# Optimization experiments

Hardware: AMD Instinct MI355X
Metric: run time of the kernel (lower is better)

## Reference

```python
import jax, jax.numpy as jnp
import numpy as np

B, T, F_IN = 32, 1664, 80
H_ENC, KV, D_DEC, EMB, VOCAB, L_DEC = 256, 128, 512, 256, 30, 200
SOS = 0  # letter2index['<sos>']


def _cell(x, h, c, Wih, Whh, b):
    # PyTorch LSTMCell gate order: i, f, g, o
    g = x @ Wih.T + h @ Whh.T + b
    i, f, gg, o = jnp.split(g, 4, axis=-1)
    c = jax.nn.sigmoid(f) * c + jax.nn.sigmoid(i) * jnp.tanh(gg)
    h = jax.nn.sigmoid(o) * jnp.tanh(c)
    return h, c


def _lstm(x, Wih, Whh, b):  # x: [B, T, D] -> [B, T, H]
    Bq, H = x.shape[0], Whh.shape[1]
    z = jnp.zeros((Bq, H), x.dtype)

    def step(hc, xt):
        h, c = _cell(xt, hc[0], hc[1], Wih, Whh, b)
        return (h, c), h

    _, hs = jax.lax.scan(step, (z, z), jnp.swapaxes(x, 0, 1))
    return jnp.swapaxes(hs, 0, 1)


def _bilstm(x, fWih, fWhh, fb, bWih, bWhh, bb):
    fw = _lstm(x, fWih, fWhh, fb)
    bw = _lstm(x[:, ::-1], bWih, bWhh, bb)[:, ::-1]
    return jnp.concatenate([fw, bw], axis=-1)


def _forward(floats, x_len, y):
    (x, e_fw_Wih, e_fw_Whh, e_fw_b, e_bw_Wih, e_bw_Whh, e_bw_b,
     p_fw_Wih, p_fw_Whh, p_fw_b, p_bw_Wih, p_bw_Whh, p_bw_b,
     Wk, bk, Wv, bv, emb, d1_Wih, d1_Whh, d1_b, d2_Wih, d2_Whh, d2_b, b_out) = floats

    # ---- Encoder: biLSTM + 3 pyramidal biLSTMs ('concat' trunc) ----
    out = _bilstm(x, e_fw_Wih, e_fw_Whh, e_fw_b, e_bw_Wih, e_bw_Whh, e_bw_b)  # [B,T,512]
    for i in range(3):
        Bn, Tn, Dn = out.shape
        out = out[:, :(Tn // 2) * 2].reshape(Bn, Tn // 2, Dn * 2)  # concat pairs of frames
        out = _bilstm(out, p_fw_Wih[i], p_fw_Whh[i], p_fw_b[i],
                      p_bw_Wih[i], p_bw_Whh[i], p_bw_b[i])
    key_ = out @ Wk.T + bk   # [B, S, KV]
    val = out @ Wv.T + bv    # [B, S, KV]
    S = key_.shape[1]

    enc_len = x_len // 8  # three halvings
    mask = jnp.arange(S)[None, :] < enc_len[:, None]  # [B, S]
    scale = 1.0 / np.sqrt(KV).astype(np.float32)

    def attend(q):  # q: [B, KV]
        e = jnp.einsum('bd,bsd->bs', q, key_) * scale
        e = jnp.where(mask, e, jnp.finfo(e.dtype).min)
        a = jax.nn.softmax(e, axis=-1)
        ctx = jnp.einsum('bs,bsd->bd', a, val)
        return ctx, a

    # ---- Decoder (train mode, teacher_forcing_rate == 1) ----
    ctx0, _ = attend(jnp.zeros((B, KV), x.dtype))
    emb_seq = emb[y]                                    # [B, L, EMB]
    sos = jnp.broadcast_to(emb[SOS], (B, EMB))
    ins = jnp.concatenate([sos[:, None], emb_seq[:, :-1]], axis=1)  # input at step t
    z1 = jnp.zeros((B, D_DEC), x.dtype)
    z2 = jnp.zeros((B, KV), x.dtype)

    def step(st, et):
        h1, c1, h2, c2, ctx = st
        yc = jnp.concatenate([et, ctx], axis=-1)
        h1, c1 = _cell(yc, h1, c1, d1_Wih, d1_Whh, d1_b)
        h2, c2 = _cell(h1, h2, c2, d2_Wih, d2_Whh, d2_b)
        ctx, a = attend(h2)
        logits = jnp.concatenate([h2, ctx], axis=-1) @ emb.T + b_out  # tied weights
        return (h1, c1, h2, c2, ctx), (logits, a[0])

    _, (logits, attn0) = jax.lax.scan(step, (z1, z1, z2, z2, ctx0), jnp.swapaxes(ins, 0, 1))
    predictions = jnp.swapaxes(logits, 0, 1)  # [B, L, VOCAB]
    return predictions, attn0                 # attn0: [L, S] (attention of sample 0)


def setup_inputs() -> dict:
    key = jax.random.key(0)
    ks = iter(jax.random.split(key, 40))

    def p(shape):
        return jax.random.normal(next(ks), shape, dtype=jnp.float32) * 0.05

    d = {
        'x': jax.random.normal(next(ks), (B, T, F_IN), dtype=jnp.float32),
        'x_len': jnp.full((B,), T, dtype=jnp.int32),
        'y': jax.random.randint(next(ks), (B, L_DEC), 0, VOCAB),
        # encoder base biLSTM (in=80, hid=256)
        'e_fw_Wih': p((4 * H_ENC, F_IN)), 'e_fw_Whh': p((4 * H_ENC, H_ENC)), 'e_fw_b': p((4 * H_ENC,)),
        'e_bw_Wih': p((4 * H_ENC, F_IN)), 'e_bw_Whh': p((4 * H_ENC, H_ENC)), 'e_bw_b': p((4 * H_ENC,)),
        # 3 pBLSTMs (in=1024 concat, hid=256), stacked on leading axis
        'p_fw_Wih': p((3, 4 * H_ENC, 4 * H_ENC)), 'p_fw_Whh': p((3, 4 * H_ENC, H_ENC)), 'p_fw_b': p((3, 4 * H_ENC)),
        'p_bw_Wih': p((3, 4 * H_ENC, 4 * H_ENC)), 'p_bw_Whh': p((3, 4 * H_ENC, H_ENC)), 'p_bw_b': p((3, 4 * H_ENC)),
        'Wk': p((KV, 2 * H_ENC)), 'bk': p((KV,)),
        'Wv': p((KV, 2 * H_ENC)), 'bv': p((KV,)),
        'emb': p((VOCAB, EMB)),  # tied with character_prob weight (EMB == 2*KV)
        'd1_Wih': p((4 * D_DEC, EMB + KV)), 'd1_Whh': p((4 * D_DEC, D_DEC)), 'd1_b': p((4 * D_DEC,)),
        'd2_Wih': p((4 * KV, D_DEC)), 'd2_Whh': p((4 * KV, KV)), 'd2_b': p((4 * KV,)),
        'b_out': p((VOCAB,)),
    }
    return d


def reference(x, e_fw_Wih, e_fw_Whh, e_fw_b, e_bw_Wih, e_bw_Whh, e_bw_b,
              p_fw_Wih, p_fw_Whh, p_fw_b, p_bw_Wih, p_bw_Whh, p_bw_b,
              Wk, bk, Wv, bv, emb, d1_Wih, d1_Whh, d1_b, d2_Wih, d2_Whh, d2_b, b_out,
              x_len, y):
    floats = (x, e_fw_Wih, e_fw_Whh, e_fw_b, e_bw_Wih, e_bw_Whh, e_bw_b,
              p_fw_Wih, p_fw_Whh, p_fw_b, p_bw_Wih, p_bw_Whh, p_bw_b,
              Wk, bk, Wv, bv, emb, d1_Wih, d1_Whh, d1_b, d2_Wih, d2_Whh, d2_b, b_out)
    return _forward(floats, x_len, y)
```

## Files before the change

kernel.cpp:

```cpp
#include <hip/hip_runtime.h>
#include <hip/hip_bf16.h>
#include <math.h>
#include <stdint.h>


#define DEV __device__ __forceinline__

#define FLAG_STRIDE 16

DEV float sigmf(float x) { return 1.0f / (1.0f + __expf(-x)); }
DEV float tanh_(float x) { return 1.0f - 2.0f / (__expf(2.0f * x) + 1.0f); }

struct __align__(8) bf4 { __hip_bfloat16 a, b, c, d; };

DEV float4 ld4g(const float* p) { return *(const float4*)p; }
DEV float4 ld4g(const __hip_bfloat16* p) {
    bf4 v = *(const bf4*)p;
    return make_float4(__bfloat162float(v.a), __bfloat162float(v.b),
                       __bfloat162float(v.c), __bfloat162float(v.d));
}
DEV void st1g(float* p, float v) { *p = v; }
DEV void st1g(__hip_bfloat16* p, float v) { *p = __float2bfloat16(v); }

DEV void st_coh(float* p, float v) {
    __hip_atomic_store(p, v, __ATOMIC_RELAXED, __HIP_MEMORY_SCOPE_AGENT);
}
DEV unsigned long long ld_coh64(const unsigned long long* p) {
    return __hip_atomic_load(p, __ATOMIC_RELAXED, __HIP_MEMORY_SCOPE_AGENT);
}
DEV float ld_coh32(const float* p) {
    return __hip_atomic_load(p, __ATOMIC_RELAXED, __HIP_MEMORY_SCOPE_AGENT);
}
DEV void st_coh64(unsigned long long* p, unsigned long long v) {
    __hip_atomic_store(p, v, __ATOMIC_RELAXED, __HIP_MEMORY_SCOPE_AGENT);
}

extern __shared__ float dyn_pad[];

DEV void step_barrier(unsigned* myflags, int w, int tid, unsigned tv)
{
    __syncthreads();
    if (tid == 0)
        __hip_atomic_store(&myflags[w * FLAG_STRIDE], tv, __ATOMIC_RELAXED,
                           __HIP_MEMORY_SCOPE_AGENT);
    if (tid < 128) {
        int guard = 0;
        while (__hip_atomic_load(&myflags[tid * FLAG_STRIDE], __ATOMIC_RELAXED,
                                 __HIP_MEMORY_SCOPE_AGENT) < tv) {
            __builtin_amdgcn_s_sleep(1);
            if (++guard > (1 << 15)) break;
        }
    }
    __syncthreads();
}

template <typename ST>
__global__ __launch_bounds__(256, 1) void lstm_l0(
    const float* __restrict__ x,
    const float* __restrict__ whh_f, const float* __restrict__ whh_b,
    const float* __restrict__ wih_f, const float* __restrict__ wih_b,
    const float* __restrict__ bias_f, const float* __restrict__ bias_b,
    ST* __restrict__ out,
    float* __restrict__ hbuf, unsigned* __restrict__ flags)
{
    const int T = 1664;
    const int RS = 388;
    __shared__ __align__(16) float hs[32 * 388];
    __shared__ float pb[4][32][9];

    const int tid = threadIdx.x;
    const int dir = blockIdx.x >> 7;
    const int w = blockIdx.x & 127;
    const int wave = tid >> 6, lane = tid & 63;
    const int cl = lane & 7;
    const int ksub = lane >> 3;
    const int slot = (wave * 8 + ksub) * 4;
    const int col = (cl >> 1) * 256 + w * 2 + (cl & 1);

    const float* Whh = dir ? whh_b : whh_f;
    const float* Wih = dir ? wih_b : wih_f;
    const float* bias = dir ? bias_b : bias_f;

    float4 wreg[3];
#pragma unroll
    for (int c = 0; c < 3; c++) {
        int k = c * 128 + slot;
        float4 v = make_float4(0.f, 0.f, 0.f, 0.f);
        if (k < 256) v = *(const float4*)&Whh[(size_t)col * 256 + k];
        else if (k - 256 < 80) v = *(const float4*)&Wih[(size_t)col * 80 + (k - 256)];
        wreg[c] = v;
    }

    const int qb = tid >> 1, qj = tid & 1;
    float bias_g[4];
#pragma unroll
    for (int g = 0; g < 4; g++) bias_g[g] = bias[g * 256 + w * 2 + (tid & 1)];
    float c_reg = 0.f;

    unsigned* myflags = flags + dir * 128 * FLAG_STRIDE;
    float* hb_base = hbuf + dir * 2 * 8192;

    for (int i = tid; i < 32 * 52; i += 256)
        hs[(i / 52) * RS + 336 + (i % 52)] = 0.f;

    for (int t = 0; t < T; t++) {
        const int par = t & 1;
        const int t_act = dir ? (T - 1 - t) : t;
        const unsigned long long* h64 =
            (const unsigned long long*)(hb_base + par * 8192);

        unsigned long long hv64[16];
#pragma unroll
        for (int j = 0; j < 16; j++)
            hv64[j] = ld_coh64(&h64[tid + j * 256]);
        float4 xf[3];
        int xn = 0;
        for (int i4 = tid; i4 < 640; i4 += 256) {
            int e = i4 * 4;
            xf[xn++] = *(const float4*)&x[((size_t)(e / 80) * 1664 + t_act) * 80 + (e % 80)];
        }
#pragma unroll
        for (int j = 0; j < 16; j++) {
            int q = tid + j * 256;
            int u = q >> 4, b0 = (q & 15) * 2;
            int uc = u ^ ((q & 7) << 2);
            hs[b0 * RS + uc] = __uint_as_float((unsigned)hv64[j]);
            hs[(b0 + 1) * RS + uc] = __uint_as_float((unsigned)(hv64[j] >> 32));
        }
        xn = 0;
        for (int i4 = tid; i4 < 640; i4 += 256) {
            int e = i4 * 4;
            *(float4*)&hs[(e / 80) * RS + 256 + (e % 80)] = xf[xn++];
        }
        __syncthreads();

        float acc[32];
#pragma unroll
        for (int b = 0; b < 32; b++) acc[b] = 0.f;
#pragma unroll
        for (int c = 0; c < 2; c++) {
            float4 wv = wreg[c];
            const int kb = c * 128 + slot;
#pragma unroll
            for (int b = 0; b < 32; b++) {
                float4 hv = *(const float4*)&hs[b * RS + (kb ^ (((b >> 1) & 7) << 2))];
                acc[b] = fmaf(hv.x, wv.x, fmaf(hv.y, wv.y, fmaf(hv.z, wv.z, fmaf(hv.w, wv.w, acc[b]))));
            }
        }
        {
            float4 wv = wreg[2];
            const float* src = &hs[256 + slot];
#pragma unroll
            for (int b = 0; b < 32; b++) {
                float4 hv = *(const float4*)&src[b * RS];
                acc[b] = fmaf(hv.x, wv.x, fmaf(hv.y, wv.y, fmaf(hv.z, wv.z, fmaf(hv.w, wv.w, acc[b]))));
            }
        }

#pragma unroll
        for (int b = 0; b < 32; b++) {
            acc[b] += __shfl_xor(acc[b], 8, 64);
            acc[b] += __shfl_xor(acc[b], 16, 64);
            acc[b] += __shfl_xor(acc[b], 32, 64);
        }
#pragma unroll
        for (int i = 0; i < 4; i++)
            pb[wave][ksub * 4 + i][cl] = acc[ksub * 4 + i];
        __syncthreads();

        if (tid < 64) {
            float ga[4];
#pragma unroll
            for (int gg = 0; gg < 4; gg++) {
                float s = bias_g[gg];
#pragma unroll
                for (int v = 0; v < 4; v++) s += pb[v][qb][gg * 2 + qj];
                ga[gg] = s;
            }
            float ci = sigmf(ga[0]), cf = sigmf(ga[1]);
            float cg = tanh_(ga[2]), co = sigmf(ga[3]);
            c_reg = cf * c_reg + ci * cg;
            float hval = co * tanh_(c_reg);
            st_coh(&hb_base[(par ^ 1) * 8192 + (w * 2 + qj) * 32 + qb], hval);
            st1g(&out[((size_t)qb * T + t_act) * 512 + dir * 256 + w * 2 + qj], hval);
        }

        step_barrier(myflags, w, tid, (unsigned)(t + 1));
    }
}

template <typename ST>
__global__ __launch_bounds__(256, 1) void lstm_pyr(
    const ST* __restrict__ in,
    const float* __restrict__ whh_f, const float* __restrict__ whh_b,
    const float* __restrict__ wih_f, const float* __restrict__ wih_b,
    const float* __restrict__ bias_f, const float* __restrict__ bias_b,
    ST* __restrict__ out,
    float* __restrict__ hbuf, unsigned* __restrict__ flags, int Tn)
{
    const int RS = 260;
    __shared__ __align__(16) float hsh[32 * 260];
    __shared__ __align__(16) float is[2][32 * 260];
    __shared__ float pb[4][32][9];

    const int tid = threadIdx.x;
    const int dir = blockIdx.x >> 7;
    const int w = blockIdx.x & 127;
    const int wave = tid >> 6, lane = tid & 63;
    const int cl = lane & 7;
    const int ksub = lane >> 3;
    const int slot = (wave * 8 + ksub) * 4;
    const int col = (cl >> 1) * 256 + w * 2 + (cl & 1);
    const int Tprev = 2 * Tn;

    const float* Whh = dir ? whh_b : whh_f;
    const float* Wih = dir ? wih_b : wih_f;
    const float* bias = dir ? bias_b : bias_f;

    float4 wreg[10];
#pragma unroll
    for (int c = 0; c < 10; c++) {
        int k = c * 128 + slot;
        wreg[c] = (k < 256)
            ? *(const float4*)&Whh[(size_t)col * 256 + k]
            : *(const float4*)&Wih[(size_t)col * 1024 + (k - 256)];
    }

    const int sb = tid >> 3, q7 = tid & 7;
    const int qb = tid >> 1, qj = tid & 1;
    float bias_g[4];
#pragma unroll
    for (int g = 0; g < 4; g++) bias_g[g] = bias[g * 256 + w * 2 + (tid & 1)];
    float c_reg = 0.f;

    unsigned* myflags = flags + dir * 128 * FLAG_STRIDE;
    float* hb_base = hbuf + dir * 2 * 8192;

    for (int t = 0; t < Tn; t++) {
        const int par = t & 1;
        const int t_act = dir ? (Tn - 1 - t) : t;
        const unsigned long long* h64 =
            (const unsigned long long*)(hb_base + par * 8192);

        float acc[32];
#pragma unroll
        for (int b = 0; b < 32; b++) acc[b] = 0.f;

        float4 gbuf[8];
        auto load_grp = [&](int g) {
            int r = 2 * t_act + (g >> 1);
            int cb = (g & 1) * 256;
            const ST* src = &in[((size_t)sb * Tprev + r) * 512 + cb + q7 * 4];
#pragma unroll
            for (int i = 0; i < 8; i++) gbuf[i] = ld4g(src + i * 32);
        };
        auto commit_grp = [&](int buf) {
#pragma unroll
            for (int i = 0; i < 8; i++)
                *(float4*)&is[buf][sb * RS + q7 * 4 + i * 32] = gbuf[i];
        };
        auto dot2 = [&](const float* base, int wi) {
#pragma unroll
            for (int cc = 0; cc < 2; cc++) {
                float4 wv = wreg[wi + cc];
                const float* src = base + cc * 128 + slot;
#pragma unroll
                for (int b = 0; b < 32; b++) {
                    float4 hv = *(const float4*)&src[b * RS];
                    acc[b] = fmaf(hv.x, wv.x, fmaf(hv.y, wv.y, fmaf(hv.z, wv.z, fmaf(hv.w, wv.w, acc[b]))));
                }
            }
        };
        auto dot2s = [&]() {
#pragma unroll
            for (int cc = 0; cc < 2; cc++) {
                float4 wv = wreg[cc];
                const int kb = cc * 128 + slot;
#pragma unroll
                for (int b = 0; b < 32; b++) {
                    float4 hv = *(const float4*)&hsh[b * RS + (kb ^ (((b >> 1) & 7) << 2))];
                    acc[b] = fmaf(hv.x, wv.x, fmaf(hv.y, wv.y, fmaf(hv.z, wv.z, fmaf(hv.w, wv.w, acc[b]))));
                }
            }
        };

        unsigned long long hv64[16];
#pragma unroll
        for (int j = 0; j < 16; j++)
            hv64[j] = ld_coh64(&h64[tid + j * 256]);
        load_grp(0);
#pragma unroll
        for (int j = 0; j < 16; j++) {
            int q = tid + j * 256;
            int u = q >> 4, b0 = (q & 15) * 2;
            int uc = u ^ ((q & 7) << 2);
            hsh[b0 * RS + uc] = __uint_as_float((unsigned)hv64[j]);
            hsh[(b0 + 1) * RS + uc] = __uint_as_float((unsigned)(hv64[j] >> 32));
        }
        commit_grp(0);
        __syncthreads();

        load_grp(1);
        dot2s();
        dot2(&is[0][0], 2);
        commit_grp(1);
        __syncthreads();

        load_grp(2);
        dot2(&is[1][0], 4);
        commit_grp(0);
        __syncthreads();

        load_grp(3);
        dot2(&is[0][0], 6);
        commit_grp(1);
        __syncthreads();

        dot2(&is[1][0], 8);

#pragma unroll
        for (int b = 0; b < 32; b++) {
            acc[b] += __shfl_xor(acc[b], 8, 64);
            acc[b] += __shfl_xor(acc[b], 16, 64);
            acc[b] += __shfl_xor(acc[b], 32, 64);
        }
#pragma unroll
        for (int i = 0; i < 4; i++)
            pb[wave][ksub * 4 + i][cl] = acc[ksub * 4 + i];
        __syncthreads();

        if (tid < 64) {
            float ga[4];
#pragma unroll
            for (int gg = 0; gg < 4; gg++) {
                float s = bias_g[gg];
#pragma unroll
                for (int v = 0; v < 4; v++) s += pb[v][qb][gg * 2 + qj];
                ga[gg] = s;
            }
            float ci = sigmf(ga[0]), cf = sigmf(ga[1]);
            float cg = tanh_(ga[2]), co = sigmf(ga[3]);
            c_reg = cf * c_reg + ci * cg;
            float hval = co * tanh_(c_reg);
            st_coh(&hb_base[(par ^ 1) * 8192 + (w * 2 + qj) * 32 + qb], hval);
            st1g(&out[((size_t)qb * Tn + t_act) * 512 + dir * 256 + w * 2 + qj], hval);
        }

        step_barrier(myflags, w, tid, (unsigned)(t + 1));
    }
}

__global__ __launch_bounds__(256) void gemm_bt(
    const float* __restrict__ A, const float* __restrict__ W,
    const float* __restrict__ bias, float* __restrict__ C,
    int M, int N, int K, int ldw)
{
    __shared__ __align__(16) float As[16][128];
    __shared__ __align__(16) float Ws[16][128];
    int tid = threadIdx.x;
    int m0 = blockIdx.x * 128, n0 = blockIdx.y * 128;
    int tx = tid & 15, ty = tid >> 4;

    float acc[8][8];
#pragma unroll
    for (int i = 0; i < 8; i++)
#pragma unroll
        for (int j = 0; j < 8; j++) acc[i][j] = 0.f;

    for (int kb = 0; kb < K; kb += 16) {
#pragma unroll
        for (int l = 0; l < 2; l++) {
            int idx = tid + l * 256;
            int row = idx >> 2, kq = (idx & 3) * 4;
            float4 v = make_float4(0.f, 0.f, 0.f, 0.f);
            if (m0 + row < M)
                v = *(const float4*)&A[(size_t)(m0 + row) * K + kb + kq];
            As[kq + 0][row] = v.x; As[kq + 1][row] = v.y;
            As[kq + 2][row] = v.z; As[kq + 3][row] = v.w;
        }
#pragma unroll
        for (int l = 0; l < 2; l++) {
            int idx = tid + l * 256;
            int row = idx >> 2, kq = (idx & 3) * 4;
            float4 v = *(const float4*)&W[(size_t)(n0 + row) * ldw + kb + kq];
            Ws[kq + 0][row] = v.x; Ws[kq + 1][row] = v.y;
            Ws[kq + 2][row] = v.z; Ws[kq + 3][row] = v.w;
        }
        __syncthreads();
#pragma unroll
        for (int k = 0; k < 16; k++) {
            float a[8], b[8];
            *(float4*)&a[0] = *(const float4*)&As[k][ty * 8];
            *(float4*)&a[4] = *(const float4*)&As[k][ty * 8 + 4];
            *(float4*)&b[0] = *(const float4*)&Ws[k][tx * 8];
            *(float4*)&b[4] = *(const float4*)&Ws[k][tx * 8 + 4];
#pragma unroll
            for (int i = 0; i < 8; i++)
#pragma unroll
                for (int j = 0; j < 8; j++)
                    acc[i][j] = fmaf(a[i], b[j], acc[i][j]);
        }
        __syncthreads();
    }
#pragma unroll
    for (int i = 0; i < 8; i++) {
        int m = m0 + ty * 8 + i;
        if (m >= M) continue;
#pragma unroll
        for (int j = 0; j < 8; j++)
            C[(size_t)m * N + n0 + tx * 8 + j] = acc[i][j] + bias[n0 + tx * 8 + j];
    }
}

__global__ void bf16_to_f32(const __hip_bfloat16* __restrict__ in,
                            float* __restrict__ out, int n)
{
    int i = blockIdx.x * 256 + threadIdx.x;
    if (i < n) out[i] = __bfloat162float(in[i]);
}

__global__ void ctx0_kernel(const float* __restrict__ val, float* __restrict__ ctxb)
{
    int gid = blockIdx.x * 256 + threadIdx.x;
    if (gid >= 4096) return;
    int k = gid >> 5, b = gid & 31;
    float s = 0.f;
    for (int t = 0; t < 208; t++) s += val[((size_t)b * 208 + t) * 128 + k];
    ctxb[b * 128 + k] = s * (1.0f / 208.0f);
}

DEV void dec_poll(unsigned* flags, int n, int tid, unsigned tv)
{
    if (tid < n) {
        int guard = 0;
        while (__hip_atomic_load(&flags[tid * FLAG_STRIDE], __ATOMIC_RELAXED,
                                 __HIP_MEMORY_SCOPE_AGENT) < tv) {
            __builtin_amdgcn_s_sleep(1);
            if (++guard > (1 << 15)) break;
        }
    }
    __syncthreads();
}

DEV void stage64k(const float* gsrc, float* dst, int tid)
{
    const unsigned long long* s64 = (const unsigned long long*)gsrc;
#pragma unroll
    for (int half = 0; half < 2; half++) {
        unsigned long long v[16];
#pragma unroll
        for (int j = 0; j < 16; j++)
            v[j] = ld_coh64(&s64[tid + (half * 16 + j) * 256]);
#pragma unroll
        for (int j = 0; j < 16; j++)
            *(unsigned long long*)&dst[2 * (tid + (half * 16 + j) * 256)] = v[j];
    }
}

DEV void stage16k(const float* gsrc, float* dst, int tid)
{
    const unsigned long long* s64 = (const unsigned long long*)gsrc;
    unsigned long long v[8];
#pragma unroll
    for (int j = 0; j < 8; j++) v[j] = ld_coh64(&s64[tid + j * 256]);
#pragma unroll
    for (int j = 0; j < 8; j++)
        *(unsigned long long*)&dst[2 * (tid + j * 256)] = v[j];
}

__global__ __launch_bounds__(256, 1) void dec_fused(
    const float* __restrict__ TBL,
    const int* __restrict__ y,
    const float* __restrict__ d1_Wih,
    const float* __restrict__ d1_Whh,
    const float* __restrict__ d2_Wih,
    const float* __restrict__ d2_Whh,
    const float* __restrict__ d2_b,
    const float* __restrict__ KEY, const float* __restrict__ VAL,
    const float* __restrict__ emb,
    const float* __restrict__ b_out,
    float* __restrict__ H1,
    float* __restrict__ H2,
    float* __restrict__ CTX,
    float* __restrict__ preds,
    float* __restrict__ attn0,
    unsigned* __restrict__ FLG)
{
    __shared__ __align__(16) float smem[36864];
    float* wA = smem;
    float* wB = smem + 16384;
    float* STG = smem + 20480;

    const int tid = threadIdx.x;
    const int blk = blockIdx.x;
    unsigned* FH1 = FLG;
    unsigned* FH2 = FLG + 64 * FLAG_STRIDE;
    unsigned* FCT = FLG + 80 * FLAG_STRIDE;

    if (blk < 64) {
        const int wg = blk;
        for (int i = tid; i < 32 * 128; i += 256) {
            int rr = i >> 7, c4 = (i & 127) * 4;
            int row = (rr >> 3) * 512 + wg * 8 + (rr & 7);
            *(float4*)&wA[rr * 512 + c4] = *(const float4*)&d1_Whh[(size_t)row * 512 + c4];
        }
        for (int i = tid; i < 32 * 32; i += 256) {
            int rr = i >> 5, c4 = (i & 31) * 4;
            int row = (rr >> 3) * 512 + wg * 8 + (rr & 7);
            *(float4*)&wB[rr * 128 + c4] = *(const float4*)&d1_Wih[(size_t)row * 384 + 256 + c4];
        }
        __syncthreads();

        const int hl = tid >> 5, b = tid & 31;
        const int h = wg * 8 + hl;
        float c1 = 0.f;
        for (int t = 0; t < 200; t++) {
            dec_poll(FH1, 64, tid, (unsigned)t);
            stage64k(H1 + (t & 1) * 16384, STG, tid);
            __syncthreads();
            int tok = (t == 0) ? 0 : y[b * 200 + t - 1];
            float acc[4];
#pragma unroll
            for (int g = 0; g < 4; g++) acc[g] = TBL[(size_t)tok * 2048 + g * 512 + h];
#pragma unroll 2
            for (int q = 0; q < 128; q++) {
                float hv0 = STG[(q * 4 + 0) * 32 + b];
                float hv1 = STG[(q * 4 + 1) * 32 + b];
                float hv2 = STG[(q * 4 + 2) * 32 + b];
                float hv3 = STG[(q * 4 + 3) * 32 + b];
#pragma unroll
                for (int g = 0; g < 4; g++) {
                    float4 w4 = *(const float4*)&wA[(g * 8 + hl) * 512 + q * 4];
                    acc[g] = fmaf(hv0, w4.x, fmaf(hv1, w4.y, fmaf(hv2, w4.z, fmaf(hv3, w4.w, acc[g]))));
                }
            }
            dec_poll(FCT, 32, tid, (unsigned)t);
            {
                const unsigned long long* s64 =
                    (const unsigned long long*)(CTX + (t & 1) * 4096);
                unsigned long long v[8];
#pragma unroll
                for (int j = 0; j < 8; j++) v[j] = ld_coh64(&s64[tid + j * 256]);
#pragma unroll
                for (int j = 0; j < 8; j++) {
                    int e = 2 * (tid + j * 256);
                    int bb = e >> 7, k = e & 127;
                    STG[bb * 130 + k] = __uint_as_float((unsigned)v[j]);
                    STG[bb * 130 + k + 1] = __uint_as_float((unsigned)(v[j] >> 32));
                }
            }
            __syncthreads();
#pragma unroll 2
            for (int q = 0; q < 32; q++) {
                float hv0 = STG[b * 130 + q * 4 + 0];
                float hv1 = STG[b * 130 + q * 4 + 1];
                float hv2 = STG[b * 130 + q * 4 + 2];
                float hv3 = STG[b * 130 + q * 4 + 3];
#pragma unroll
                for (int g = 0; g < 4; g++) {
                    float4 w4 = *(const float4*)&wB[(g * 8 + hl) * 128 + q * 4];
                    acc[g] = fmaf(hv0, w4.x, fmaf(hv1, w4.y, fmaf(hv2, w4.z, fmaf(hv3, w4.w, acc[g]))));
                }
            }
            float ci = sigmf(acc[0]), cf = sigmf(acc[1]);
            float cg = tanh_(acc[2]), co = sigmf(acc[3]);
            c1 = cf * c1 + ci * cg;
            float hval = co * tanh_(c1);
            st_coh(&H1[((t + 1) & 1) * 16384 + h * 32 + b], hval);
            __syncthreads();
            if (tid == 0)
                __hip_atomic_store(&FH1[wg * FLAG_STRIDE], (unsigned)(t + 1),
                                   __ATOMIC_RELAXED, __HIP_MEMORY_SCOPE_AGENT);
        }
    } else if (blk < 80) {
        const int wg = blk - 64;
        for (int i = tid; i < 32 * 128; i += 256) {
            int rr = i >> 7, c4 = (i & 127) * 4;
            int row = (rr >> 3) * 128 + wg * 8 + (rr & 7);
            *(float4*)&wA[rr * 512 + c4] = *(const float4*)&d2_Wih[(size_t)row * 512 + c4];
        }
        for (int i = tid; i < 32 * 32; i += 256) {
            int rr = i >> 5, c4 = (i & 31) * 4;
            int row = (rr >> 3) * 128 + wg * 8 + (rr & 7);
            *(float4*)&wB[rr * 128 + c4] = *(const float4*)&d2_Whh[(size_t)row * 128 + c4];
        }
        __syncthreads();

        const int hl = tid >> 5, b = tid & 31;
        const int h = wg * 8 + hl;
        float bias_r[4];
#pragma unroll
        for (int g = 0; g < 4; g++) bias_r[g] = d2_b[g * 128 + h];
        float c2 = 0.f;
        for (int t = 0; t < 200; t++) {
            dec_poll(FH2, 16, tid, (unsigned)t);
            stage16k(H2 + (t & 1) * 4096, STG, tid);
            __syncthreads();
            float acc[4];
#pragma unroll
            for (int g = 0; g < 4; g++) acc[g] = bias_r[g];
#pragma unroll 2
            for (int q = 0; q < 32; q++) {
                float hv0 = STG[(q * 4 + 0) * 32 + b];
                float hv1 = STG[(q * 4 + 1) * 32 + b];
                float hv2 = STG[(q * 4 + 2) * 32 + b];
                float hv3 = STG[(q * 4 + 3) * 32 + b];
#pragma unroll
                for (int g = 0; g < 4; g++) {
                    float4 w4 = *(const float4*)&wB[(g * 8 + hl) * 128 + q * 4];
                    acc[g] = fmaf(hv0, w4.x, fmaf(hv1, w4.y, fmaf(hv2, w4.z, fmaf(hv3, w4.w, acc[g]))));
                }
            }
            dec_poll(FH1, 64, tid, (unsigned)(t + 1));
            stage64k(H1 + ((t + 1) & 1) * 16384, STG, tid);
            __syncthreads();
#pragma unroll 2
            for (int q = 0; q < 128; q++) {
                float hv0 = STG[(q * 4 + 0) * 32 + b];
                float hv1 = STG[(q * 4 + 1) * 32 + b];
                float hv2 = STG[(q * 4 + 2) * 32 + b];
                float hv3 = STG[(q * 4 + 3) * 32 + b];
#pragma unroll
                for (int g = 0; g < 4; g++) {
                    float4 w4 = *(const float4*)&wA[(g * 8 + hl) * 512 + q * 4];
                    acc[g] = fmaf(hv0, w4.x, fmaf(hv1, w4.y, fmaf(hv2, w4.z, fmaf(hv3, w4.w, acc[g]))));
                }
            }
            float ci = sigmf(acc[0]), cf = sigmf(acc[1]);
            float cg = tanh_(acc[2]), co = sigmf(acc[3]);
            c2 = cf * c2 + ci * cg;
            float hval = co * tanh_(c2);
            st_coh(&H2[((t + 1) & 1) * 4096 + h * 32 + b], hval);
            __syncthreads();
            if (tid == 0)
                __hip_atomic_store(&FH2[wg * FLAG_STRIDE], (unsigned)(t + 1),
                                   __ATOMIC_RELAXED, __HIP_MEMORY_SCOPE_AGENT);
        }
    } else {
        const int b = blk - 80;
        const int lane = tid & 63, wv = tid >> 6;
        float* qv    = STG;
        float* ctx_s = STG + 128;
        float* av    = STG + 256;
        float* redA  = STG + 512;
        float* redB  = STG + 520;
        float* red2  = STG + 640;

        for (int t = 0; t < 200; t++) {
            dec_poll(FH2, 16, tid, (unsigned)(t + 1));
            const float* h2b = H2 + ((t + 1) & 1) * 4096;
            if (tid < 128) qv[tid] = ld_coh32(&h2b[tid * 32 + b]);
            __syncthreads();

            float e = -INFINITY;
            if (tid < 208) {
                float s = 0.f;
                const float* kr = KEY + ((size_t)b * 208 + tid) * 128;
#pragma unroll
                for (int qd = 0; qd < 32; qd++) {
                    float4 k4 = *(const float4*)&kr[qd * 4];
                    float4 q4 = *(const float4*)&qv[qd * 4];
                    s = fmaf(k4.x, q4.x, fmaf(k4.y, q4.y, fmaf(k4.z, q4.z, fmaf(k4.w, q4.w, s))));
                }
                e = s * 0.08838834764831845f;
            }
            float m = e;
#pragma unroll
            for (int off = 32; off >= 1; off >>= 1)
                m = fmaxf(m, __shfl_xor(m, off, 64));
            if (lane == 0) redA[wv] = m;
            __syncthreads();
            m = fmaxf(fmaxf(redA[0], redA[1]), fmaxf(redA[2], redA[3]));
            float ex = (tid < 208) ? __expf(e - m) : 0.f;
            float sm = ex;
#pragma unroll
            for (int off = 32; off >= 1; off >>= 1)
                sm += __shfl_xor(sm, off, 64);
            if (lane == 0) redB[wv] = sm;
            __syncthreads();
            float inv = 1.0f / (redB[0] + redB[1] + redB[2] + redB[3]);
            if (tid < 208) av[tid] = ex * inv;
            if (b == 0 && tid < 208) attn0[t * 208 + tid] = ex * inv;
            __syncthreads();

            {
                int k = tid & 127, sh = tid >> 7;
                const float* vb = VAL + (size_t)b * 208 * 128 + k;
                int sbase = sh * 104;
                float s0 = 0.f, s1 = 0.f;
#pragma unroll 4
                for (int ss = 0; ss < 104; ss += 2) {
                    s0 = fmaf(av[sbase + ss],     vb[(size_t)(sbase + ss) * 128], s0);
                    s1 = fmaf(av[sbase + ss + 1], vb[(size_t)(sbase + ss + 1) * 128], s1);
                }
                s0 += s1;
                if (sh == 1) red2[k] = s0;
                __syncthreads();
                if (sh == 0) ctx_s[k] = s0 + red2[k];
            }
            __syncthreads();

            if (tid < 64) {
                unsigned long long u =
                    ((unsigned long long)__float_as_uint(ctx_s[2 * tid + 1]) << 32) |
                    __float_as_uint(ctx_s[2 * tid]);
                st_coh64((unsigned long long*)&CTX[((t + 1) & 1) * 4096 + b * 128 + 2 * tid], u);
            }
            if (tid < 30) {
                const float* er = emb + tid * 256;
                float s = b_out[tid];
#pragma unroll 4
                for (int kk = 0; kk < 32; kk++) {
                    float4 e4 = *(const float4*)&er[kk * 4];
                    float4 q4 = *(const float4*)&qv[kk * 4];
                    s = fmaf(e4.x, q4.x, fmaf(e4.y, q4.y, fmaf(e4.z, q4.z, fmaf(e4.w, q4.w, s))));
                }
#pragma unroll 4
                for (int kk = 0; kk < 32; kk++) {
                    float4 e4 = *(const float4*)&er[128 + kk * 4];
                    float4 c4 = *(const float4*)&ctx_s[kk * 4];
                    s = fmaf(e4.x, c4.x, fmaf(e4.y, c4.y, fmaf(e4.z, c4.z, fmaf(e4.w, c4.w, s))));
                }
                preds[((size_t)b * 200 + t) * 30 + tid] = s;
            }
            __syncthreads();
            if (tid == 0)
                __hip_atomic_store(&FCT[b * FLAG_STRIDE], (unsigned)(t + 1),
                                   __ATOMIC_RELAXED, __HIP_MEMORY_SCOPE_AGENT);
        }
    }
}

template <typename ST>
static void run_encoder(const float* x,
                        const float* e_fw_Wih, const float* e_fw_Whh, const float* e_fw_b,
                        const float* e_bw_Wih, const float* e_bw_Whh, const float* e_bw_b,
                        const float* p_fw_Wih, const float* p_fw_Whh, const float* p_fw_b,
                        const float* p_bw_Wih, const float* p_bw_Whh, const float* p_bw_b,
                        ST* A, ST* B, float* HB, unsigned* FLG, hipStream_t stream)
{
    hipMemsetAsync(HB, 0, 32768 * 4, stream);
    hipMemsetAsync(FLG, 0, 2 * 128 * FLAG_STRIDE * 4, stream);
    hipLaunchKernelGGL((lstm_l0<ST>), dim3(256), dim3(256), 32 * 1024, stream,
                       x, e_fw_Whh, e_bw_Whh, e_fw_Wih, e_bw_Wih, e_fw_b, e_bw_b,
                       A, HB, FLG);

    int Ts[3] = {832, 416, 208};
    const ST* ins[3] = {A, B, A};
    ST* outs[3] = {B, A, B};
    for (int L = 0; L < 3; L++) {
        hipMemsetAsync(HB, 0, 32768 * 4, stream);
        hipMemsetAsync(FLG, 0, 2 * 128 * FLAG_STRIDE * 4, stream);
        hipLaunchKernelGGL((lstm_pyr<ST>), dim3(256), dim3(256), 0, stream,
                           ins[L],
                           p_fw_Whh + (size_t)L * 1024 * 256, p_bw_Whh + (size_t)L * 1024 * 256,
                           p_fw_Wih + (size_t)L * 1024 * 1024, p_bw_Wih + (size_t)L * 1024 * 1024,
                           p_fw_b + L * 1024, p_bw_b + L * 1024,
                           outs[L], HB, FLG, Ts[L]);
    }
}

extern "C" void kernel_launch(void* const* d_in, const int* in_sizes, int n_in,
                              void* d_out, int out_size, void* d_ws, size_t ws_size,
                              hipStream_t stream)
{
    const float* x        = (const float*)d_in[0];
    const int*   y        = (const int*)d_in[2];
    const float* e_fw_Wih = (const float*)d_in[3];
    const float* e_fw_Whh = (const float*)d_in[4];
    const float* e_fw_b   = (const float*)d_in[5];
    const float* e_bw_Wih = (const float*)d_in[6];
    const float* e_bw_Whh = (const float*)d_in[7];
    const float* e_bw_b   = (const float*)d_in[8];
    const float* p_fw_Wih = (const float*)d_in[9];
    const float* p_fw_Whh = (const float*)d_in[10];
    const float* p_fw_b   = (const float*)d_in[11];
    const float* p_bw_Wih = (const float*)d_in[12];
    const float* p_bw_Whh = (const float*)d_in[13];
    const float* p_bw_b   = (const float*)d_in[14];
    const float* Wk       = (const float*)d_in[15];
    const float* bk       = (const float*)d_in[16];
    const float* Wv       = (const float*)d_in[17];
    const float* bv       = (const float*)d_in[18];
    const float* emb      = (const float*)d_in[19];
    const float* d1_Wih   = (const float*)d_in[20];
    const float* d1_Whh   = (const float*)d_in[21];
    const float* d1_b     = (const float*)d_in[22];
    const float* d2_Wih   = (const float*)d_in[23];
    const float* d2_Whh   = (const float*)d_in[24];
    const float* d2_b     = (const float*)d_in[25];
    const float* b_out    = (const float*)d_in[26];

    char* base = (char*)d_ws;
    size_t off = 0;
    auto alloc = [&](size_t bytes) -> void* {
        void* p = base + off;
        off = (off + bytes + 255) & ~(size_t)255;
        return p;
    };

    float*    KEY = (float*)alloc(851968ull * 4);
    float*    VAL = (float*)alloc(851968ull * 4);
    float*    TBL = (float*)alloc(61440ull * 4);
    float*    HB  = (float*)alloc(32768ull * 4);
    unsigned* FLG = (unsigned*)alloc(2 * 128 * FLAG_STRIDE * 4);
    float*    H1  = (float*)alloc(32768ull * 4);
    float*    H2  = (float*)alloc(8192ull * 4);
    float*    CTX = (float*)alloc(8192ull * 4);

    const size_t A_elems = 32ull * 1664 * 512;
    const size_t B_elems = 32ull * 832 * 512;
    const size_t L3_elems = 32ull * 208 * 512;

    size_t misc_end = off;
    size_t need_f32  = misc_end + (A_elems + B_elems) * 4 + 2048;
    size_t need_bf16 = misc_end + L3_elems * 4 + (A_elems + B_elems) * 2 + 2048;

    const float* enc_out;
    if (ws_size >= need_f32) {
        float* A = (float*)alloc(A_elems * 4);
        float* B = (float*)alloc(B_elems * 4);
        run_encoder<float>(x, e_fw_Wih, e_fw_Whh, e_fw_b, e_bw_Wih, e_bw_Whh, e_bw_b,
                           p_fw_Wih, p_fw_Whh, p_fw_b, p_bw_Wih, p_bw_Whh, p_bw_b,
                           A, B, HB, FLG, stream);
        enc_out = B;
    } else if (ws_size >= need_bf16) {
        float* CONV = (float*)alloc(L3_elems * 4);
        __hip_bfloat16* A = (__hip_bfloat16*)alloc(A_elems * 2);
        __hip_bfloat16* B = (__hip_bfloat16*)alloc(B_elems * 2);
        run_encoder<__hip_bfloat16>(x, e_fw_Wih, e_fw_Whh, e_fw_b, e_bw_Wih, e_bw_Whh, e_bw_b,
                                    p_fw_Wih, p_fw_Whh, p_fw_b, p_bw_Wih, p_bw_Whh, p_bw_b,
                                    A, B, HB, FLG, stream);
        hipLaunchKernelGGL(bf16_to_f32, dim3((unsigned)(L3_elems / 256)), dim3(256), 0, stream,
                           B, CONV, (int)L3_elems);
        enc_out = CONV;
    } else {
        return;
    }

    hipLaunchKernelGGL(gemm_bt, dim3(52, 1), dim3(256), 0, stream,
                       enc_out, Wk, bk, KEY, 6656, 128, 512, 512);
    hipLaunchKernelGGL(gemm_bt, dim3(52, 1), dim3(256), 0, stream,
                       enc_out, Wv, bv, VAL, 6656, 128, 512, 512);
    hipLaunchKernelGGL(gemm_bt, dim3(1, 16), dim3(256), 0, stream,
                       emb, d1_Wih, d1_b, TBL, 30, 2048, 256, 384);
    hipLaunchKernelGGL(ctx0_kernel, dim3(16), dim3(256), 0, stream, VAL, CTX);
    hipMemsetAsync(H1, 0, 32768 * 4, stream);
    hipMemsetAsync(H2, 0, 8192 * 4, stream);
    hipMemsetAsync(FLG, 0, 2 * 128 * FLAG_STRIDE * 4, stream);

    float* preds = (float*)d_out;
    float* attn0 = (float*)d_out + 192000;

    hipLaunchKernelGGL(dec_fused, dim3(112), dim3(256), 0, stream,
                       TBL, y, d1_Wih, d1_Whh, d2_Wih, d2_Whh, d2_b,
                       KEY, VAL, emb, b_out, H1, H2, CTX, preds, attn0, FLG);
}
```

Baseline: 33.72 ms.

## Replace grid-synchronized layer-0 LSTM with per-batch-pair blocks streaming transposed weights

The first encoder biLSTM no longer splits gate columns across 256 cooperating blocks that meet at a global flag barrier every timestep. It now launches 32 independent 1024-thread blocks, each owning two batch rows of one direction, so every step needs only block-local syncs. A prep kernel first rearranges the concatenated Whh/Wih weights into a float4-interleaved layout for coalesced loads. The cost is that each block re-reads about 1.4MB of weights from L2 every timestep instead of keeping them in registers, and only 32 CUs do the work.

```diff
diff --git a/kernel.cpp b/kernel.cpp
--- a/kernel.cpp
+++ b/kernel.cpp
@@ -34,8 +34,6 @@
 DEV void st_coh64(unsigned long long* p, unsigned long long v) {
     __hip_atomic_store(p, v, __ATOMIC_RELAXED, __HIP_MEMORY_SCOPE_AGENT);
 }
-
-extern __shared__ float dyn_pad[];
 
 DEV void step_barrier(unsigned* myflags, int w, int tid, unsigned tv)
 {
@@ -54,138 +52,78 @@
     __syncthreads();
 }
 
+__global__ void wt4_prep(const float* __restrict__ whh_f, const float* __restrict__ whh_b,
+                         const float* __restrict__ wih_f, const float* __restrict__ wih_b,
+                         float* __restrict__ WT4)
+{
+    int idx = blockIdx.x * 256 + threadIdx.x;
+    if (idx >= 688128) return;
+    int j = idx & 3, r = (idx >> 2) & 1023, kc = (idx >> 12) % 84, d = idx / 344064;
+    int k = kc * 4 + j;
+    const float* Whh = d ? whh_b : whh_f;
+    const float* Wih = d ? wih_b : wih_f;
+    float v = (k < 256) ? Whh[r * 256 + k] : Wih[r * 80 + (k - 256)];
+    WT4[idx] = v;
+}
+
 template <typename ST>
-__global__ __launch_bounds__(256, 1) void lstm_l0(
+__global__ __launch_bounds__(1024, 1) void lstm_l0_bp(
     const float* __restrict__ x,
-    const float* __restrict__ whh_f, const float* __restrict__ whh_b,
-    const float* __restrict__ wih_f, const float* __restrict__ wih_b,
+    const float* __restrict__ WT4,
     const float* __restrict__ bias_f, const float* __restrict__ bias_b,
-    ST* __restrict__ out,
-    float* __restrict__ hbuf, unsigned* __restrict__ flags)
+    ST* __restrict__ out)
 {
     const int T = 1664;
-    const int RS = 388;
-    __shared__ __align__(16) float hs[32 * 388];
-    __shared__ float pb[4][32][9];
+    __shared__ __align__(16) float hx[2][344];
+    __shared__ float gs[2][1024];
 
     const int tid = threadIdx.x;
-    const int dir = blockIdx.x >> 7;
-    const int w = blockIdx.x & 127;
-    const int wave = tid >> 6, lane = tid & 63;
-    const int cl = lane & 7;
-    const int ksub = lane >> 3;
-    const int slot = (wave * 8 + ksub) * 4;
-    const int col = (cl >> 1) * 256 + w * 2 + (cl & 1);
-
-    const float* Whh = dir ? whh_b : whh_f;
-    const float* Wih = dir ? wih_b : wih_f;
-    const float* bias = dir ? bias_b : bias_f;
-
-    float4 wreg[3];
-#pragma unroll
-    for (int c = 0; c < 3; c++) {
-        int k = c * 128 + slot;
-        float4 v = make_float4(0.f, 0.f, 0.f, 0.f);
-        if (k < 256) v = *(const float4*)&Whh[(size_t)col * 256 + k];
-        else if (k - 256 < 80) v = *(const float4*)&Wih[(size_t)col * 80 + (k - 256)];
-        wreg[c] = v;
-    }
-
-    const int qb = tid >> 1, qj = tid & 1;
-    float bias_g[4];
-#pragma unroll
-    for (int g = 0; g < 4; g++) bias_g[g] = bias[g * 256 + w * 2 + (tid & 1)];
+    const int d = blockIdx.x & 1;
+    const int b0 = (blockIdx.x >> 1) * 2;
+
+    const float* Wbase = WT4 + (size_t)d * 344064;
+    const float bias_r = (d ? bias_b : bias_f)[tid];
     float c_reg = 0.f;
 
-    unsigned* myflags = flags + dir * 128 * FLAG_STRIDE;
-    float* hb_base = hbuf + dir * 2 * 8192;
-
-    for (int i = tid; i < 32 * 52; i += 256)
-        hs[(i / 52) * RS + 336 + (i % 52)] = 0.f;
+    if (tid < 688) {
+        int s = tid >= 344;
+        hx[s][tid - s * 344] = 0.f;
+    }
+    __syncthreads();
 
     for (int t = 0; t < T; t++) {
-        const int par = t & 1;
-        const int t_act = dir ? (T - 1 - t) : t;
-        const unsigned long long* h64 =
-            (const unsigned long long*)(hb_base + par * 8192);
-
-        unsigned long long hv64[16];
-#pragma unroll
-        for (int j = 0; j < 16; j++)
-            hv64[j] = ld_coh64(&h64[tid + j * 256]);
-        float4 xf[3];
-        int xn = 0;
-        for (int i4 = tid; i4 < 640; i4 += 256) {
-            int e = i4 * 4;
-            xf[xn++] = *(const float4*)&x[((size_t)(e / 80) * 1664 + t_act) * 80 + (e % 80)];
-        }
-#pragma unroll
-        for (int j = 0; j < 16; j++) {
-            int q = tid + j * 256;
-            int u = q >> 4, b0 = (q & 15) * 2;
-            int uc = u ^ ((q & 7) << 2);
-            hs[b0 * RS + uc] = __uint_as_float((unsigned)hv64[j]);
-            hs[(b0 + 1) * RS + uc] = __uint_as_float((unsigned)(hv64[j] >> 32));
-        }
-        xn = 0;
-        for (int i4 = tid; i4 < 640; i4 += 256) {
-            int e = i4 * 4;
-            *(float4*)&hs[(e / 80) * RS + 256 + (e % 80)] = xf[xn++];
-        }
-        __syncthreads();
-
-        float acc[32];
-#pragma unroll
-        for (int b = 0; b < 32; b++) acc[b] = 0.f;
-#pragma unroll
-        for (int c = 0; c < 2; c++) {
-            float4 wv = wreg[c];
-            const int kb = c * 128 + slot;
-#pragma unroll
-            for (int b = 0; b < 32; b++) {
-                float4 hv = *(const float4*)&hs[b * RS + (kb ^ (((b >> 1) & 7) << 2))];
-                acc[b] = fmaf(hv.x, wv.x, fmaf(hv.y, wv.y, fmaf(hv.z, wv.z, fmaf(hv.w, wv.w, acc[b]))));
-            }
-        }
-        {
-            float4 wv = wreg[2];
-            const float* src = &hs[256 + slot];
-#pragma unroll
-            for (int b = 0; b < 32; b++) {
-                float4 hv = *(const float4*)&src[b * RS];
-                acc[b] = fmaf(hv.x, wv.x, fmaf(hv.y, wv.y, fmaf(hv.z, wv.z, fmaf(hv.w, wv.w, acc[b]))));
-            }
-        }
-
-#pragma unroll
-        for (int b = 0; b < 32; b++) {
-            acc[b] += __shfl_xor(acc[b], 8, 64);
-            acc[b] += __shfl_xor(acc[b], 16, 64);
-            acc[b] += __shfl_xor(acc[b], 32, 64);
-        }
-#pragma unroll
-        for (int i = 0; i < 4; i++)
-            pb[wave][ksub * 4 + i][cl] = acc[ksub * 4 + i];
-        __syncthreads();
-
-        if (tid < 64) {
-            float ga[4];
-#pragma unroll
-            for (int gg = 0; gg < 4; gg++) {
-                float s = bias_g[gg];
-#pragma unroll
-                for (int v = 0; v < 4; v++) s += pb[v][qb][gg * 2 + qj];
-                ga[gg] = s;
-            }
-            float ci = sigmf(ga[0]), cf = sigmf(ga[1]);
-            float cg = tanh_(ga[2]), co = sigmf(ga[3]);
+        const int t_act = d ? (T - 1 - t) : t;
+
+        if (tid < 40) {
+            int s = tid / 20, j = tid % 20;
+            *(float4*)&hx[s][256 + j * 4] =
+                *(const float4*)&x[((size_t)(b0 + s) * T + t_act) * 80 + j * 4];
+        }
+        __syncthreads();
+
+        float a0 = bias_r, a1 = bias_r;
+#pragma unroll 4
+        for (int kc = 0; kc < 84; kc++) {
+            float4 w4 = *(const float4*)&Wbase[(size_t)(kc * 1024 + tid) * 4];
+            float4 h0 = *(const float4*)&hx[0][kc * 4];
+            float4 h1 = *(const float4*)&hx[1][kc * 4];
+            a0 = fmaf(w4.x, h0.x, fmaf(w4.y, h0.y, fmaf(w4.z, h0.z, fmaf(w4.w, h0.w, a0))));
+            a1 = fmaf(w4.x, h1.x, fmaf(w4.y, h1.y, fmaf(w4.z, h1.z, fmaf(w4.w, h1.w, a1))));
+        }
+        gs[0][tid] = a0;
+        gs[1][tid] = a1;
+        __syncthreads();
+
+        if (tid < 512) {
+            int s = tid >> 8, uu = tid & 255;
+            float gi = gs[s][uu], gf = gs[s][256 + uu];
+            float gg = gs[s][512 + uu], go = gs[s][768 + uu];
+            float ci = sigmf(gi), cf = sigmf(gf), cg = tanh_(gg), co = sigmf(go);
             c_reg = cf * c_reg + ci * cg;
             float hval = co * tanh_(c_reg);
-            st_coh(&hb_base[(par ^ 1) * 8192 + (w * 2 + qj) * 32 + qb], hval);
-            st1g(&out[((size_t)qb * T + t_act) * 512 + dir * 256 + w * 2 + qj], hval);
-        }
-
-        step_barrier(myflags, w, tid, (unsigned)(t + 1));
+            hx[s][uu] = hval;
+            st1g(&out[((size_t)(b0 + s) * T + t_act) * 512 + d * 256 + uu], hval);
+        }
     }
 }
 
@@ -737,13 +675,13 @@
                         const float* e_bw_Wih, const float* e_bw_Whh, const float* e_bw_b,
                         const float* p_fw_Wih, const float* p_fw_Whh, const float* p_fw_b,
                         const float* p_bw_Wih, const float* p_bw_Whh, const float* p_bw_b,
-                        ST* A, ST* B, float* HB, unsigned* FLG, hipStream_t stream)
-{
-    hipMemsetAsync(HB, 0, 32768 * 4, stream);
-    hipMemsetAsync(FLG, 0, 2 * 128 * FLAG_STRIDE * 4, stream);
-    hipLaunchKernelGGL((lstm_l0<ST>), dim3(256), dim3(256), 32 * 1024, stream,
-                       x, e_fw_Whh, e_bw_Whh, e_fw_Wih, e_bw_Wih, e_fw_b, e_bw_b,
-                       A, HB, FLG);
+                        ST* A, ST* B, float* HB, unsigned* FLG, float* WT4,
+                        hipStream_t stream)
+{
+    hipLaunchKernelGGL(wt4_prep, dim3(2688), dim3(256), 0, stream,
+                       e_fw_Whh, e_bw_Whh, e_fw_Wih, e_bw_Wih, WT4);
+    hipLaunchKernelGGL((lstm_l0_bp<ST>), dim3(32), dim3(1024), 0, stream,
+                       x, WT4, e_fw_b, e_bw_b, A);
 
     int Ts[3] = {832, 416, 208};
     const ST* ins[3] = {A, B, A};
@@ -807,6 +745,7 @@
     float*    H1  = (float*)alloc(32768ull * 4);
     float*    H2  = (float*)alloc(8192ull * 4);
     float*    CTX = (float*)alloc(8192ull * 4);
+    float*    WT4 = (float*)alloc(688128ull * 4);
 
     const size_t A_elems = 32ull * 1664 * 512;
     const size_t B_elems = 32ull * 832 * 512;
@@ -822,7 +761,7 @@
         float* B = (float*)alloc(B_elems * 4);
         run_encoder<float>(x, e_fw_Wih, e_fw_Whh, e_fw_b, e_bw_Wih, e_bw_Whh, e_bw_b,
                            p_fw_Wih, p_fw_Whh, p_fw_b, p_bw_Wih, p_bw_Whh, p_bw_b,
-                           A, B, HB, FLG, stream);
+                           A, B, HB, FLG, WT4, stream);
         enc_out = B;
     } else if (ws_size >= need_bf16) {
         float* CONV = (float*)alloc(L3_elems * 4);
@@ -830,7 +769,7 @@
         __hip_bfloat16* B = (__hip_bfloat16*)alloc(B_elems * 2);
         run_encoder<__hip_bfloat16>(x, e_fw_Wih, e_fw_Whh, e_fw_b, e_bw_Wih, e_bw_Whh, e_bw_b,
                                     p_fw_Wih, p_fw_Whh, p_fw_b, p_bw_Wih, p_bw_Whh, p_bw_b,
-                                    A, B, HB, FLG, stream);
+                                    A, B, HB, FLG, WT4, stream);
         hipLaunchKernelGGL(bf16_to_f32, dim3((unsigned)(L3_elems / 256)), dim3(256), 0, stream,
                            B, CONV, (int)L3_elems);
         enc_out = CONV;
```

Result: slower. 39.47 ms (+17.1%).
